# Kernel tuning notes

Measured on AMD Instinct MI355X. Metric: run time of the kernel, lower is better.

## Reference

```python
import jax, jax.numpy as jnp
import numpy as np

H = 16          # num_heads
D = 1024        # in_features
NH = D // H     # per-head dim
EPS = 1e-5


def _ln(x, g, b):
    m = jnp.mean(x, axis=-1, keepdims=True)
    v = jnp.mean((x - m) ** 2, axis=-1, keepdims=True)
    return (x - m) / jnp.sqrt(v + EPS) * g + b


def _mha(q, k, v, Wq, bq, Wk, bk, Wv, bv, causal):
    # q: [Tq,B,D], k/v: [Tk,B,D]
    Tq, B, _ = q.shape
    Tk = k.shape[0]
    qh = (q @ Wq + bq).reshape(Tq, B, H, NH)
    kh = (k @ Wk + bk).reshape(Tk, B, H, NH)
    vh = (v @ Wv + bv).reshape(Tk, B, H, NH)
    scale = 1.0 / np.float32(np.sqrt(NH))
    logits = jnp.einsum('qbhd,kbhd->bhqk', qh, kh) * scale  # [B,H,Tq,Tk]
    if causal:
        mask = jnp.tril(jnp.ones((Tq, Tk), dtype=bool))
        logits = jnp.where(mask, logits, -jnp.inf)  # softmax over prefix [0..t]
    w = jax.nn.softmax(logits, axis=-1)
    out = jnp.einsum('bhqk,kbhd->qbhd', w, vh).reshape(Tq, B, D)
    return out


def setup_inputs() -> dict:
    key = jax.random.key(0)
    ks = jax.random.split(key, 12)
    s = 0.02
    T, B = 1024, 8
    inp = {
        'encoder_input': jax.random.normal(ks[0], (T, B, D), jnp.float32),
        'decoder_input': jax.random.normal(ks[1], (T, B, D), jnp.float32),
        # self-attention projections
        'Wq1': jax.random.normal(ks[2], (D, D), jnp.float32) * s,
        'bq1': jnp.zeros((D,), jnp.float32),
        'Wk1': jax.random.normal(ks[3], (D, D), jnp.float32) * s,
        'bk1': jnp.zeros((D,), jnp.float32),
        'Wv1': jax.random.normal(ks[4], (D, D), jnp.float32) * s,
        'bv1': jnp.zeros((D,), jnp.float32),
        # cross-attention projections
        'Wq2': jax.random.normal(ks[5], (D, D), jnp.float32) * s,
        'bq2': jnp.zeros((D,), jnp.float32),
        'Wk2': jax.random.normal(ks[6], (D, D), jnp.float32) * s,
        'bk2': jnp.zeros((D,), jnp.float32),
        'Wv2': jax.random.normal(ks[7], (D, D), jnp.float32) * s,
        'bv2': jnp.zeros((D,), jnp.float32),
        # position-wise linear
        'Wl': jax.random.normal(ks[8], (D, D), jnp.float32) * s,
        'bl': jnp.zeros((D,), jnp.float32),
        # layernorms
        'g1': jnp.ones((D,), jnp.float32), 'be1': jnp.zeros((D,), jnp.float32),
        'g2': jnp.ones((D,), jnp.float32), 'be2': jnp.zeros((D,), jnp.float32),
        'g3': jnp.ones((D,), jnp.float32), 'be3': jnp.zeros((D,), jnp.float32),
    }
    return inp


def reference(encoder_input, decoder_input,
              Wq1, bq1, Wk1, bk1, Wv1, bv1,
              Wq2, bq2, Wk2, bk2, Wv2, bv2,
              Wl, bl, g1, be1, g2, be2, g3, be3):
    # causal self-attention (prefix [:t+1] per step == causal mask)
    x = _mha(decoder_input, decoder_input, decoder_input,
             Wq1, bq1, Wk1, bk1, Wv1, bv1, causal=True)
    x = _ln(x + decoder_input, g1, be1)
    # cross-attention over full encoder input
    y = _mha(x, encoder_input, encoder_input,
             Wq2, bq2, Wk2, bk2, Wv2, bv2, causal=False)
    y = _ln(y + x, g2, be2)
    # position-wise linear (no activation in source) + residual + LN
    z = y @ Wl + bl
    out = _ln(z + y, g3, be3)
    return out
```

## Files before the change

kernel.cpp:

```cpp
#include <hip/hip_runtime.h>
#include <hip/hip_bf16.h>

typedef __bf16 bf16x8 __attribute__((ext_vector_type(8)));
typedef float f32x4 __attribute__((ext_vector_type(4)));

#define MFMA16(A, B, C) __builtin_amdgcn_mfma_f32_16x16x32_bf16(A, B, C, 0, 0, 0)

#define GLDS(gp, lp)                                                              \
    __builtin_amdgcn_global_load_lds(                                             \
        (const __attribute__((address_space(1))) void*)(gp),                      \
        (__attribute__((address_space(3))) void*)(lp), 16, 0, 0)

struct PtrW { const float* p[7]; };
__global__ __launch_bounds__(256) void wt_transpose(PtrW W, __hip_bfloat16* __restrict__ Wt) {
    const float* __restrict__ src = W.p[blockIdx.z];
    __hip_bfloat16* __restrict__ dst = Wt + ((size_t)blockIdx.z << 20);
    __shared__ float tile[32][33];
    const int bn = blockIdx.x * 32;
    const int bk = blockIdx.y * 32;
    const int tx = threadIdx.x, ty = threadIdx.y;
#pragma unroll
    for (int i = 0; i < 4; i++) {
        tile[ty + i * 8][tx] = src[(size_t)(bk + ty + i * 8) * 1024 + bn + tx];
    }
    __syncthreads();
#pragma unroll
    for (int i = 0; i < 4; i++) {
        dst[(size_t)(bn + ty + i * 8) * 1024 + bk + tx] =
            __float2bfloat16(tile[tx][ty + i * 8]);
    }
}

struct PtrC { const float* s[2]; __hip_bfloat16* d[2]; };
__global__ __launch_bounds__(256) void to_bf16(PtrC c) {
    const int z = blockIdx.y;
    const int i = (blockIdx.x * 256 + threadIdx.x) * 4;
    const float4 v = *(const float4*)(c.s[z] + i);
    __align__(8) __hip_bfloat16 t[4] = {__float2bfloat16(v.x), __float2bfloat16(v.y),
                                        __float2bfloat16(v.z), __float2bfloat16(v.w)};
    *(uint2*)(c.d[z] + i) = *(const uint2*)t;
}

struct Ptr2 { const float* p[2]; };
__global__ __launch_bounds__(256) void bias_concat(Ptr2 srcs, float* __restrict__ dst) {
    const int i = threadIdx.x * 4;
    *(float4*)(dst + blockIdx.x * 1024 + i) = *(const float4*)(srcs.p[blockIdx.x] + i);
}

struct Job {
    const __hip_bfloat16* A;
    const __hip_bfloat16* B;
    const float* bias;
    __hip_bfloat16* out;
    int bstride;
    int N;
    int nblocks;
    int gx;
    float qscale;
    int qcols;
};
struct Jobs { Job j[4]; int njobs; };

__global__ __launch_bounds__(256) void gemm_multi(Jobs J) {
    int bid = blockIdx.x;
    int ji = 0;
    while (ji < J.njobs - 1 && bid >= J.j[ji].nblocks) {
        bid -= J.j[ji].nblocks;
        ji++;
    }
    const Job job = J.j[ji];
    int bx, by, bb;
    if (job.N) {
        bx = bid % job.gx;
        by = bid / job.gx;
        bb = 0;
    } else {
        bx = bid & 7;
        by = (bid >> 3) & 7;
        bb = bid >> 6;
    }
    __shared__ __align__(16) __hip_bfloat16 As[2][128 * 32];
    __shared__ __align__(16) __hip_bfloat16 Bs[2][128 * 32];
    const int tid = threadIdx.x;
    const int wave = tid >> 6, lane = tid & 63;
    const int quad = lane >> 4, l16 = lane & 15;
    const int m0 = bx * 128, n0 = by * 128;
    const int wm = (wave & 1) * 64, wn = (wave >> 1) * 64;
    const int srow = lane >> 2;
    const int lc = (lane & 3) ^ ((lane >> 3) & 3);
    const __hip_bfloat16* Bbase = job.B + (job.N ? 0 : bb * 1024);
    const __hip_bfloat16* ap[2];
    const __hip_bfloat16* bp[2];
    int loff[2];
#pragma unroll
    for (int u = 0; u < 2; u++) {
        const int g = wave * 2 + u;
        const int row = g * 16 + srow;
        ap[u] = job.A + (size_t)(m0 + row) * 1024 + lc * 8;
        bp[u] = Bbase + (size_t)(n0 + row) * job.bstride + lc * 8;
        loff[u] = g * 512;
    }
    const int pch = quad ^ ((l16 >> 1) & 3);
    f32x4 acc[4][4] = {};
#pragma unroll
    for (int u = 0; u < 2; u++) {
        GLDS(ap[u], &As[0][loff[u]]);
        GLDS(bp[u], &Bs[0][loff[u]]);
    }
    int sel = 0;
    for (int k0 = 0; k0 < 1024; k0 += 32) {
        __syncthreads();
        if (k0 + 32 < 1024) {
#pragma unroll
            for (int u = 0; u < 2; u++) {
                GLDS(ap[u] + k0 + 32, &As[sel ^ 1][loff[u]]);
                GLDS(bp[u] + k0 + 32, &Bs[sel ^ 1][loff[u]]);
            }
        }
        bf16x8 af[4], bfr[4];
#pragma unroll
        for (int i = 0; i < 4; i++) {
            af[i] = *(const bf16x8*)(&As[sel][(wm + i * 16 + l16) * 32 + pch * 8]);
            bfr[i] = *(const bf16x8*)(&Bs[sel][(wn + i * 16 + l16) * 32 + pch * 8]);
        }
#pragma unroll
        for (int i = 0; i < 4; i++)
#pragma unroll
            for (int j = 0; j < 4; j++)
                acc[i][j] = MFMA16(af[i], bfr[j], acc[i][j]);
        sel ^= 1;
    }
    if (job.N) {
#pragma unroll
        for (int i = 0; i < 4; i++) {
#pragma unroll
            for (int j = 0; j < 4; j++) {
                const int mr = m0 + wm + i * 16 + quad * 4;
                const int nc = n0 + wn + j * 16 + l16;
                const float sc = (nc < job.qcols) ? job.qscale : 1.0f;
                const float bv = job.bias[nc];
#pragma unroll
                for (int r = 0; r < 4; r++) {
                    const float v = (acc[i][j][r] + bv) * sc;
                    job.out[(size_t)(mr + r) * job.N + nc] = __float2bfloat16(v);
                }
            }
        }
    } else {
#pragma unroll
        for (int i = 0; i < 4; i++) {
            const int mr = m0 + wm + i * 16 + quad * 4;
            float bias_r[4];
#pragma unroll
            for (int r = 0; r < 4; r++) bias_r[r] = job.bias[mr + r];
#pragma unroll
            for (int j = 0; j < 4; j++) {
                const int nc = n0 + wn + j * 16 + l16;
#pragma unroll
                for (int r = 0; r < 4; r++) {
                    const int d = mr + r;
                    const size_t idx = ((size_t)bb << 20) + ((size_t)(d >> 6) << 16) +
                                       (size_t)(d & 63) * 1024 + nc;
                    job.out[idx] = __float2bfloat16(acc[i][j][r] + bias_r[r]);
                }
            }
        }
    }
}

__global__ __launch_bounds__(256) void attn_kernel(
    const __hip_bfloat16* __restrict__ Qp, const __hip_bfloat16* __restrict__ Kp,
    const __hip_bfloat16* __restrict__ Vt, __hip_bfloat16* __restrict__ Ob,
    int T, int qRS, int kRS, int causal) {
    __shared__ __align__(16) __hip_bfloat16 Ks[2][64 * 64];
    __shared__ __align__(16) __hip_bfloat16 Vs[2][64 * 64];
    __shared__ __align__(16) __hip_bfloat16 Ps[4][16 * 64];
    const int tid = threadIdx.x, wave = tid >> 6, lane = tid & 63;
    const int quad = lane >> 4, l16 = lane & 15;
    const int gid = blockIdx.x;
    const int bh = (gid & 7) * 16 + ((gid >> 3) & 15);
    const int qt = gid >> 7;
    const int b = bh & 7, h = bh >> 3;
    const int q0 = qt * 128;
    const int qstride = 8 * qRS, kstride = 8 * kRS;
    const int sw = l16 & 7;

    const int qg0 = q0 + wave * 16;
    const int qg1 = qg0 + 64;
    const int myq0 = qg0 + l16, myq1 = qg1 + l16;
    const __hip_bfloat16* qbase = Qp + (size_t)b * qRS + h * 64;
    const bf16x8 qf00 = *(const bf16x8*)(qbase + (size_t)myq0 * qstride + quad * 8);
    const bf16x8 qf01 = *(const bf16x8*)(qbase + (size_t)myq0 * qstride + 32 + quad * 8);
    const bf16x8 qf10 = *(const bf16x8*)(qbase + (size_t)myq1 * qstride + quad * 8);
    const bf16x8 qf11 = *(const bf16x8*)(qbase + (size_t)myq1 * qstride + 32 + quad * 8);
    bf16x8 onesf;
#pragma unroll
    for (int i = 0; i < 8; i++) onesf[i] = (__bf16)1.0f;

    const int jk = wave * 2;
    const int lrow = lane >> 3;
    const int lch = (lane & 7) ^ (lrow & 7);
    const __hip_bfloat16* kp0 =
        Kp + (size_t)b * kRS + h * 64 + (size_t)(jk * 8 + lrow) * kstride + lch * 8;
    const __hip_bfloat16* kp1 = kp0 + (size_t)8 * kstride;
    const __hip_bfloat16* vp0 =
        Vt + ((size_t)(b * 16 + h) << 16) + (size_t)(jk * 8 + lrow) * 1024 + lch * 8;
    const __hip_bfloat16* vp1 = vp0 + 8 * 1024;
    const size_t kinc = (size_t)64 * kstride;

    f32x4 o0[4] = {}, o1[4] = {};
    f32x4 ol0 = {}, ol1 = {};
    bf16x8 pf00, pf01, pf10, pf11;

    auto softmax = [&](f32x4* s, f32x4& ol, bf16x8& pf0, bf16x8& pf1, int qg, int myq,
                       int k0) {
        const bool nm = causal && (k0 + 63 > qg);
        if (nm) {
#pragma unroll
            for (int n = 0; n < 4; n++)
#pragma unroll
                for (int r = 0; r < 4; r++)
                    if (k0 + n * 16 + quad * 4 + r > myq) s[n][r] = -1e30f;
        }
#pragma unroll
        for (int n = 0; n < 4; n++) {
            const float p0 = __builtin_amdgcn_exp2f(s[n][0]);
            const float p1 = __builtin_amdgcn_exp2f(s[n][1]);
            const float p2 = __builtin_amdgcn_exp2f(s[n][2]);
            const float p3 = __builtin_amdgcn_exp2f(s[n][3]);
            const __hip_bfloat162 pa = __float22bfloat162_rn(make_float2(p0, p1));
            const __hip_bfloat162 pb = __float22bfloat162_rn(make_float2(p2, p3));
            uint2 w;
            w.x = *(const unsigned int*)&pa;
            w.y = *(const unsigned int*)&pb;
            const int gcp = 2 * n + (quad >> 1);
            *(uint2*)(&Ps[wave][l16 * 64 + ((gcp ^ sw) << 3) + (quad & 1) * 4]) = w;
        }
        pf0 = *(const bf16x8*)(&Ps[wave][l16 * 64 + ((quad ^ sw) << 3)]);
        pf1 = *(const bf16x8*)(&Ps[wave][l16 * 64 + (((quad + 4) ^ sw) << 3)]);
        ol = MFMA16(onesf, pf0, ol);
        ol = MFMA16(onesf, pf1, ol);
    };

    const int kend = causal ? (q0 + 128) : T;
    GLDS(kp0, &Ks[0][jk * 512]);
    GLDS(kp1, &Ks[0][jk * 512 + 512]);
    GLDS(vp0, &Vs[0][jk * 512]);
    GLDS(vp1, &Vs[0][jk * 512 + 512]);
    const __hip_bfloat16* kn0 = kp0 + kinc;
    const __hip_bfloat16* kn1 = kp1 + kinc;
    const __hip_bfloat16* vn0 = vp0 + 64;
    const __hip_bfloat16* vn1 = vp1 + 64;
    int sel = 0;
    for (int k0 = 0; k0 < kend; k0 += 64) {
        __syncthreads();
        if (k0 + 64 < kend) {
            GLDS(kn0, &Ks[sel ^ 1][jk * 512]);
            GLDS(kn1, &Ks[sel ^ 1][jk * 512 + 512]);
            GLDS(vn0, &Vs[sel ^ 1][jk * 512]);
            GLDS(vn1, &Vs[sel ^ 1][jk * 512 + 512]);
            kn0 += kinc; kn1 += kinc; vn0 += 64; vn1 += 64;
        }
        const bool act0 = !causal || (k0 <= qg0 + 15);
        f32x4 s0[4] = {}, s1[4] = {};
        {
            bf16x8 kf[4];
#pragma unroll
            for (int n = 0; n < 4; n++)
                kf[n] = *(const bf16x8*)(&Ks[sel][(n * 16 + l16) * 64 +
                                                  ((quad ^ sw) << 3)]);
#pragma unroll
            for (int n = 0; n < 4; n++) {
                if (act0) s0[n] = MFMA16(kf[n], qf00, s0[n]);
                s1[n] = MFMA16(kf[n], qf10, s1[n]);
            }
#pragma unroll
            for (int n = 0; n < 4; n++)
                kf[n] = *(const bf16x8*)(&Ks[sel][(n * 16 + l16) * 64 +
                                                  (((quad + 4) ^ sw) << 3)]);
#pragma unroll
            for (int n = 0; n < 4; n++) {
                if (act0) s0[n] = MFMA16(kf[n], qf01, s0[n]);
                s1[n] = MFMA16(kf[n], qf11, s1[n]);
            }
        }
        if (act0) softmax(s0, ol0, pf00, pf01, qg0, myq0, k0);
        softmax(s1, ol1, pf10, pf11, qg1, myq1, k0);
#pragma unroll
        for (int mm = 0; mm < 4; mm++) {
            const int vrow = (mm * 16 + l16) * 64;
            const bf16x8 vf0 = *(const bf16x8*)(&Vs[sel][vrow + ((quad ^ sw) << 3)]);
            const bf16x8 vf1 = *(const bf16x8*)(&Vs[sel][vrow + (((quad + 4) ^ sw) << 3)]);
            if (act0) {
                o0[mm] = MFMA16(vf0, pf00, o0[mm]);
                o0[mm] = MFMA16(vf1, pf01, o0[mm]);
            }
            o1[mm] = MFMA16(vf0, pf10, o1[mm]);
            o1[mm] = MFMA16(vf1, pf11, o1[mm]);
        }
        sel ^= 1;
    }
    const float inv0 = 1.0f / ol0[0];
    const float inv1 = 1.0f / ol1[0];
    __hip_bfloat16* ob0 = Ob + (size_t)b * 1024 + h * 64 + (size_t)myq0 * 8192;
    __hip_bfloat16* ob1 = Ob + (size_t)b * 1024 + h * 64 + (size_t)myq1 * 8192;
#pragma unroll
    for (int mm = 0; mm < 4; mm++) {
        __align__(8) __hip_bfloat16 t0[4] = {
            __float2bfloat16(o0[mm][0] * inv0), __float2bfloat16(o0[mm][1] * inv0),
            __float2bfloat16(o0[mm][2] * inv0), __float2bfloat16(o0[mm][3] * inv0)};
        *(uint2*)(ob0 + mm * 16 + quad * 4) = *(const uint2*)t0;
        __align__(8) __hip_bfloat16 t1[4] = {
            __float2bfloat16(o1[mm][0] * inv1), __float2bfloat16(o1[mm][1] * inv1),
            __float2bfloat16(o1[mm][2] * inv1), __float2bfloat16(o1[mm][3] * inv1)};
        *(uint2*)(ob1 + mm * 16 + quad * 4) = *(const uint2*)t1;
    }
}

__global__ __launch_bounds__(256) void ln_res_kernel(
    const __hip_bfloat16* __restrict__ a, const float* __restrict__ resf,
    const __hip_bfloat16* __restrict__ resb, const float* __restrict__ g,
    const float* __restrict__ be, float* __restrict__ outf,
    __hip_bfloat16* __restrict__ outb) {
    const int tid = threadIdx.x, wave = tid >> 6, lane = tid & 63;
    const int row = blockIdx.x * 4 + wave;
    const size_t base = (size_t)row * 1024;
    float x[16];
#pragma unroll
    for (int c = 0; c < 4; c++) {
        const int off = c * 256 + lane * 4;
        const uint2 ar = *(const uint2*)(a + base + off);
        const __hip_bfloat16* ah = (const __hip_bfloat16*)&ar;
        if (resf) {
            const float4 rv = *(const float4*)(resf + base + off);
            x[c * 4 + 0] = __bfloat162float(ah[0]) + rv.x;
            x[c * 4 + 1] = __bfloat162float(ah[1]) + rv.y;
            x[c * 4 + 2] = __bfloat162float(ah[2]) + rv.z;
            x[c * 4 + 3] = __bfloat162float(ah[3]) + rv.w;
        } else {
            const uint2 br = *(const uint2*)(resb + base + off);
            const __hip_bfloat16* bhp = (const __hip_bfloat16*)&br;
#pragma unroll
            for (int k = 0; k < 4; k++)
                x[c * 4 + k] = __bfloat162float(ah[k]) + __bfloat162float(bhp[k]);
        }
    }
    float s = 0.f, ss = 0.f;
#pragma unroll
    for (int k = 0; k < 16; k++) {
        s += x[k];
        ss += x[k] * x[k];
    }
#pragma unroll
    for (int w = 32; w >= 1; w >>= 1) {
        s += __shfl_xor(s, w);
        ss += __shfl_xor(ss, w);
    }
    const float mean = s * (1.f / 1024.f);
    const float inv = rsqrtf(ss * (1.f / 1024.f) - mean * mean + 1e-5f);
#pragma unroll
    for (int c = 0; c < 4; c++) {
        const int off = c * 256 + lane * 4;
        const float4 gg = *(const float4*)(g + off);
        const float4 bb = *(const float4*)(be + off);
        float y[4];
        y[0] = (x[c * 4 + 0] - mean) * inv * gg.x + bb.x;
        y[1] = (x[c * 4 + 1] - mean) * inv * gg.y + bb.y;
        y[2] = (x[c * 4 + 2] - mean) * inv * gg.z + bb.z;
        y[3] = (x[c * 4 + 3] - mean) * inv * gg.w + bb.w;
        if (outf) *(float4*)(outf + base + off) = make_float4(y[0], y[1], y[2], y[3]);
        if (outb) {
            __align__(8) __hip_bfloat16 t[4] = {
                __float2bfloat16(y[0]), __float2bfloat16(y[1]),
                __float2bfloat16(y[2]), __float2bfloat16(y[3])};
            *(uint2*)(outb + base + off) = *(const uint2*)t;
        }
    }
}

extern "C" void kernel_launch(void* const* d_in, const int* in_sizes, int n_in,
                              void* d_out, int out_size, void* d_ws, size_t ws_size,
                              hipStream_t stream) {
    const float* enc = (const float*)d_in[0];
    const float* dec = (const float*)d_in[1];
    const float* Wq1 = (const float*)d_in[2];
    const float* bq1 = (const float*)d_in[3];
    const float* Wk1 = (const float*)d_in[4];
    const float* bk1 = (const float*)d_in[5];
    const float* Wv1 = (const float*)d_in[6];
    const float* bv1 = (const float*)d_in[7];
    const float* Wq2 = (const float*)d_in[8];
    const float* bq2 = (const float*)d_in[9];
    const float* Wk2 = (const float*)d_in[10];
    const float* bk2 = (const float*)d_in[11];
    const float* Wv2 = (const float*)d_in[12];
    const float* bv2 = (const float*)d_in[13];
    const float* Wl = (const float*)d_in[14];
    const float* bl = (const float*)d_in[15];
    const float* g1 = (const float*)d_in[16];
    const float* be1 = (const float*)d_in[17];
    const float* g2 = (const float*)d_in[18];
    const float* be2 = (const float*)d_in[19];
    const float* g3 = (const float*)d_in[20];
    const float* be3 = (const float*)d_in[21];
    float* outp = (float*)d_out;

    char* p = (char*)d_ws;
    auto alloc = [&](size_t n) {
        char* r = p;
        p += (n + 255) & ~(size_t)255;
        return r;
    };
    const size_t MD = (size_t)8192 * 1024;
    __hip_bfloat16* enc_b = (__hip_bfloat16*)alloc(MD * 2);
    __hip_bfloat16* dec_b = (__hip_bfloat16*)alloc(MD * 2);
    __hip_bfloat16* Wt = (__hip_bfloat16*)alloc((size_t)7 * 1024 * 1024 * 2);
    float* bcat = (float*)alloc(2048 * sizeof(float));
    __hip_bfloat16* qk = (__hip_bfloat16*)alloc(MD * 2 * 2);
    __hip_bfloat16* k2b = (__hip_bfloat16*)alloc(MD * 2);
    __hip_bfloat16* qb = (__hip_bfloat16*)alloc(MD * 2);
    __hip_bfloat16* attnb = (__hip_bfloat16*)alloc(MD * 2);
    __hip_bfloat16* Vtb = (__hip_bfloat16*)alloc(MD * 2);
    __hip_bfloat16* Vtb2 = (__hip_bfloat16*)alloc(MD * 2);
    __hip_bfloat16* xb = dec_b;
    __hip_bfloat16* yb = enc_b;

    const float QSC = 0.18033688f;

    PtrW wptrs = {{Wq1, Wk1, Wv1, Wq2, Wk2, Wv2, Wl}};
    wt_transpose<<<dim3(32, 32, 7), dim3(32, 8), 0, stream>>>(wptrs, Wt);
    PtrC cp = {{enc, dec}, {enc_b, dec_b}};
    to_bf16<<<dim3(8192, 2), 256, 0, stream>>>(cp);
    Ptr2 bp = {{bq1, bk1}};
    bias_concat<<<2, 256, 0, stream>>>(bp, bcat);

    {
        Jobs J;
        J.j[0] = {dec_b, Wt, bcat, qk, 1024, 2048, 64 * 16, 64, QSC, 1024};
        J.j[1] = {Wt + ((size_t)2 << 20), dec_b, bv1, Vtb, 8192, 0, 512, 8, 1.0f, 0};
        J.j[2] = {enc_b, Wt + ((size_t)4 << 20), bk2, k2b, 1024, 1024, 64 * 8, 64, 1.0f, 0};
        J.j[3] = {Wt + ((size_t)5 << 20), enc_b, bv2, Vtb2, 8192, 0, 512, 8, 1.0f, 0};
        J.njobs = 4;
        gemm_multi<<<2560, 256, 0, stream>>>(J);
    }

    attn_kernel<<<1024, 256, 0, stream>>>(qk, qk + 1024, Vtb, attnb,
                                          1024, 2048, 2048, 1);
    ln_res_kernel<<<2048, 256, 0, stream>>>(attnb, dec, nullptr, g1, be1, nullptr, xb);

    {
        Jobs J;
        J.j[0] = {xb, Wt + ((size_t)3 << 20), bq2, qb, 1024, 1024, 64 * 8, 64, QSC, 1024};
        J.njobs = 1;
        gemm_multi<<<512, 256, 0, stream>>>(J);
    }
    attn_kernel<<<1024, 256, 0, stream>>>(qb, k2b, Vtb2, attnb, 1024, 1024, 1024, 0);
    ln_res_kernel<<<2048, 256, 0, stream>>>(attnb, nullptr, xb, g2, be2, nullptr, yb);

    {
        Jobs J;
        J.j[0] = {yb, Wt + ((size_t)6 << 20), bl, qb, 1024, 1024, 64 * 8, 64, 1.0f, 0};
        J.njobs = 1;
        gemm_multi<<<512, 256, 0, stream>>>(J);
    }
    ln_res_kernel<<<2048, 256, 0, stream>>>(qb, nullptr, yb, g3, be3, outp, nullptr);
}
```

Baseline: 524.2 us.

## Pair causal query tiles per block and move cross-attn K/V GEMMs later

Result: faster. 499.4 us (-4.7%).

```diff
diff --git a/kernel.cpp b/kernel.cpp
--- a/kernel.cpp
+++ b/kernel.cpp
@@ -59,7 +59,7 @@
     float qscale;
     int qcols;
 };
-struct Jobs { Job j[4]; int njobs; };
+struct Jobs { Job j[3]; int njobs; };
 
 __global__ __launch_bounds__(256) void gemm_multi(Jobs J) {
     int bid = blockIdx.x;
@@ -171,7 +171,7 @@
 __global__ __launch_bounds__(256) void attn_kernel(
     const __hip_bfloat16* __restrict__ Qp, const __hip_bfloat16* __restrict__ Kp,
     const __hip_bfloat16* __restrict__ Vt, __hip_bfloat16* __restrict__ Ob,
-    int T, int qRS, int kRS, int causal) {
+    int T, int qRS, int kRS, int causal, int paired) {
     __shared__ __align__(16) __hip_bfloat16 Ks[2][64 * 64];
     __shared__ __align__(16) __hip_bfloat16 Vs[2][64 * 64];
     __shared__ __align__(16) __hip_bfloat16 Ps[4][16 * 64];
@@ -179,141 +179,146 @@
     const int quad = lane >> 4, l16 = lane & 15;
     const int gid = blockIdx.x;
     const int bh = (gid & 7) * 16 + ((gid >> 3) & 15);
-    const int qt = gid >> 7;
+    const int sid = gid >> 7;
     const int b = bh & 7, h = bh >> 3;
-    const int q0 = qt * 128;
     const int qstride = 8 * qRS, kstride = 8 * kRS;
     const int sw = l16 & 7;
-
-    const int qg0 = q0 + wave * 16;
-    const int qg1 = qg0 + 64;
-    const int myq0 = qg0 + l16, myq1 = qg1 + l16;
-    const __hip_bfloat16* qbase = Qp + (size_t)b * qRS + h * 64;
-    const bf16x8 qf00 = *(const bf16x8*)(qbase + (size_t)myq0 * qstride + quad * 8);
-    const bf16x8 qf01 = *(const bf16x8*)(qbase + (size_t)myq0 * qstride + 32 + quad * 8);
-    const bf16x8 qf10 = *(const bf16x8*)(qbase + (size_t)myq1 * qstride + quad * 8);
-    const bf16x8 qf11 = *(const bf16x8*)(qbase + (size_t)myq1 * qstride + 32 + quad * 8);
-    bf16x8 onesf;
-#pragma unroll
-    for (int i = 0; i < 8; i++) onesf[i] = (__bf16)1.0f;
-
     const int jk = wave * 2;
     const int lrow = lane >> 3;
     const int lch = (lane & 7) ^ (lrow & 7);
-    const __hip_bfloat16* kp0 =
+    const __hip_bfloat16* qbase = Qp + (size_t)b * qRS + h * 64;
+    const __hip_bfloat16* kbase =
         Kp + (size_t)b * kRS + h * 64 + (size_t)(jk * 8 + lrow) * kstride + lch * 8;
-    const __hip_bfloat16* kp1 = kp0 + (size_t)8 * kstride;
-    const __hip_bfloat16* vp0 =
+    const __hip_bfloat16* vbase =
         Vt + ((size_t)(b * 16 + h) << 16) + (size_t)(jk * 8 + lrow) * 1024 + lch * 8;
-    const __hip_bfloat16* vp1 = vp0 + 8 * 1024;
     const size_t kinc = (size_t)64 * kstride;
-
-    f32x4 o0[4] = {}, o1[4] = {};
-    f32x4 ol0 = {}, ol1 = {};
-    bf16x8 pf00, pf01, pf10, pf11;
-
-    auto softmax = [&](f32x4* s, f32x4& ol, bf16x8& pf0, bf16x8& pf1, int qg, int myq,
-                       int k0) {
-        const bool nm = causal && (k0 + 63 > qg);
-        if (nm) {
-#pragma unroll
-            for (int n = 0; n < 4; n++)
-#pragma unroll
-                for (int r = 0; r < 4; r++)
-                    if (k0 + n * 16 + quad * 4 + r > myq) s[n][r] = -1e30f;
-        }
-#pragma unroll
-        for (int n = 0; n < 4; n++) {
-            const float p0 = __builtin_amdgcn_exp2f(s[n][0]);
-            const float p1 = __builtin_amdgcn_exp2f(s[n][1]);
-            const float p2 = __builtin_amdgcn_exp2f(s[n][2]);
-            const float p3 = __builtin_amdgcn_exp2f(s[n][3]);
-            const __hip_bfloat162 pa = __float22bfloat162_rn(make_float2(p0, p1));
-            const __hip_bfloat162 pb = __float22bfloat162_rn(make_float2(p2, p3));
-            uint2 w;
-            w.x = *(const unsigned int*)&pa;
-            w.y = *(const unsigned int*)&pb;
-            const int gcp = 2 * n + (quad >> 1);
-            *(uint2*)(&Ps[wave][l16 * 64 + ((gcp ^ sw) << 3) + (quad & 1) * 4]) = w;
-        }
-        pf0 = *(const bf16x8*)(&Ps[wave][l16 * 64 + ((quad ^ sw) << 3)]);
-        pf1 = *(const bf16x8*)(&Ps[wave][l16 * 64 + (((quad + 4) ^ sw) << 3)]);
-        ol = MFMA16(onesf, pf0, ol);
-        ol = MFMA16(onesf, pf1, ol);
-    };
-
-    const int kend = causal ? (q0 + 128) : T;
-    GLDS(kp0, &Ks[0][jk * 512]);
-    GLDS(kp1, &Ks[0][jk * 512 + 512]);
-    GLDS(vp0, &Vs[0][jk * 512]);
-    GLDS(vp1, &Vs[0][jk * 512 + 512]);
-    const __hip_bfloat16* kn0 = kp0 + kinc;
-    const __hip_bfloat16* kn1 = kp1 + kinc;
-    const __hip_bfloat16* vn0 = vp0 + 64;
-    const __hip_bfloat16* vn1 = vp1 + 64;
-    int sel = 0;
-    for (int k0 = 0; k0 < kend; k0 += 64) {
-        __syncthreads();
-        if (k0 + 64 < kend) {
-            GLDS(kn0, &Ks[sel ^ 1][jk * 512]);
-            GLDS(kn1, &Ks[sel ^ 1][jk * 512 + 512]);
-            GLDS(vn0, &Vs[sel ^ 1][jk * 512]);
-            GLDS(vn1, &Vs[sel ^ 1][jk * 512 + 512]);
-            kn0 += kinc; kn1 += kinc; vn0 += 64; vn1 += 64;
-        }
-        const bool act0 = !causal || (k0 <= qg0 + 15);
-        f32x4 s0[4] = {}, s1[4] = {};
-        {
-            bf16x8 kf[4];
-#pragma unroll
-            for (int n = 0; n < 4; n++)
-                kf[n] = *(const bf16x8*)(&Ks[sel][(n * 16 + l16) * 64 +
-                                                  ((quad ^ sw) << 3)]);
+    bf16x8 onesf;
+#pragma unroll
+    for (int i = 0; i < 8; i++) onesf[i] = (__bf16)1.0f;
+
+    const int nrep = paired ? 2 : 1;
+    for (int rep = 0; rep < nrep; rep++) {
+        const int qt = paired ? (rep ? sid : 7 - sid) : sid;
+        const int q0 = qt * 128;
+        const int qg0 = q0 + wave * 16;
+        const int qg1 = qg0 + 64;
+        const int myq0 = qg0 + l16, myq1 = qg1 + l16;
+        const bf16x8 qf00 = *(const bf16x8*)(qbase + (size_t)myq0 * qstride + quad * 8);
+        const bf16x8 qf01 =
+            *(const bf16x8*)(qbase + (size_t)myq0 * qstride + 32 + quad * 8);
+        const bf16x8 qf10 = *(const bf16x8*)(qbase + (size_t)myq1 * qstride + quad * 8);
+        const bf16x8 qf11 =
+            *(const bf16x8*)(qbase + (size_t)myq1 * qstride + 32 + quad * 8);
+
+        f32x4 o0[4] = {}, o1[4] = {};
+        f32x4 ol0 = {}, ol1 = {};
+        bf16x8 pf00, pf01, pf10, pf11;
+
+        auto softmax = [&](f32x4* s, f32x4& ol, bf16x8& pf0, bf16x8& pf1, int qg,
+                           int myq, int k0) {
+            const bool nm = causal && (k0 + 63 > qg);
+            if (nm) {
+#pragma unroll
+                for (int n = 0; n < 4; n++)
+#pragma unroll
+                    for (int r = 0; r < 4; r++)
+                        if (k0 + n * 16 + quad * 4 + r > myq) s[n][r] = -1e30f;
+            }
 #pragma unroll
             for (int n = 0; n < 4; n++) {
-                if (act0) s0[n] = MFMA16(kf[n], qf00, s0[n]);
-                s1[n] = MFMA16(kf[n], qf10, s1[n]);
-            }
-#pragma unroll
-            for (int n = 0; n < 4; n++)
-                kf[n] = *(const bf16x8*)(&Ks[sel][(n * 16 + l16) * 64 +
-                                                  (((quad + 4) ^ sw) << 3)]);
-#pragma unroll
-            for (int n = 0; n < 4; n++) {
-                if (act0) s0[n] = MFMA16(kf[n], qf01, s0[n]);
-                s1[n] = MFMA16(kf[n], qf11, s1[n]);
-            }
-        }
-        if (act0) softmax(s0, ol0, pf00, pf01, qg0, myq0, k0);
-        softmax(s1, ol1, pf10, pf11, qg1, myq1, k0);
+                const float p0 = __builtin_amdgcn_exp2f(s[n][0]);
+                const float p1 = __builtin_amdgcn_exp2f(s[n][1]);
+                const float p2 = __builtin_amdgcn_exp2f(s[n][2]);
+                const float p3 = __builtin_amdgcn_exp2f(s[n][3]);
+                const __hip_bfloat162 pa = __float22bfloat162_rn(make_float2(p0, p1));
+                const __hip_bfloat162 pb = __float22bfloat162_rn(make_float2(p2, p3));
+                uint2 w;
+                w.x = *(const unsigned int*)&pa;
+                w.y = *(const unsigned int*)&pb;
+                const int gcp = 2 * n + (quad >> 1);
+                *(uint2*)(&Ps[wave][l16 * 64 + ((gcp ^ sw) << 3) + (quad & 1) * 4]) = w;
+            }
+            pf0 = *(const bf16x8*)(&Ps[wave][l16 * 64 + ((quad ^ sw) << 3)]);
+            pf1 = *(const bf16x8*)(&Ps[wave][l16 * 64 + (((quad + 4) ^ sw) << 3)]);
+            ol = MFMA16(onesf, pf0, ol);
+            ol = MFMA16(onesf, pf1, ol);
+        };
+
+        const int kend = causal ? (q0 + 128) : T;
+        if (rep) __syncthreads();
+        GLDS(kbase, &Ks[0][jk * 512]);
+        GLDS(kbase + (size_t)8 * kstride, &Ks[0][jk * 512 + 512]);
+        GLDS(vbase, &Vs[0][jk * 512]);
+        GLDS(vbase + 8 * 1024, &Vs[0][jk * 512 + 512]);
+        const __hip_bfloat16* kn0 = kbase + kinc;
+        const __hip_bfloat16* kn1 = kbase + (size_t)8 * kstride + kinc;
+        const __hip_bfloat16* vn0 = vbase + 64;
+        const __hip_bfloat16* vn1 = vbase + 8 * 1024 + 64;
+        int sel = 0;
+        for (int k0 = 0; k0 < kend; k0 += 64) {
+            __syncthreads();
+            if (k0 + 64 < kend) {
+                GLDS(kn0, &Ks[sel ^ 1][jk * 512]);
+                GLDS(kn1, &Ks[sel ^ 1][jk * 512 + 512]);
+                GLDS(vn0, &Vs[sel ^ 1][jk * 512]);
+                GLDS(vn1, &Vs[sel ^ 1][jk * 512 + 512]);
+                kn0 += kinc; kn1 += kinc; vn0 += 64; vn1 += 64;
+            }
+            const bool act0 = !causal || (k0 <= qg0 + 15);
+            f32x4 s0[4] = {}, s1[4] = {};
+            {
+                bf16x8 kf[4];
+#pragma unroll
+                for (int n = 0; n < 4; n++)
+                    kf[n] = *(const bf16x8*)(&Ks[sel][(n * 16 + l16) * 64 +
+                                                      ((quad ^ sw) << 3)]);
+#pragma unroll
+                for (int n = 0; n < 4; n++) {
+                    if (act0) s0[n] = MFMA16(kf[n], qf00, s0[n]);
+                    s1[n] = MFMA16(kf[n], qf10, s1[n]);
+                }
+#pragma unroll
+                for (int n = 0; n < 4; n++)
+                    kf[n] = *(const bf16x8*)(&Ks[sel][(n * 16 + l16) * 64 +
+                                                      (((quad + 4) ^ sw) << 3)]);
+#pragma unroll
+                for (int n = 0; n < 4; n++) {
+                    if (act0) s0[n] = MFMA16(kf[n], qf01, s0[n]);
+                    s1[n] = MFMA16(kf[n], qf11, s1[n]);
+                }
+            }
+            if (act0) softmax(s0, ol0, pf00, pf01, qg0, myq0, k0);
+            softmax(s1, ol1, pf10, pf11, qg1, myq1, k0);
+#pragma unroll
+            for (int mm = 0; mm < 4; mm++) {
+                const int vrow = (mm * 16 + l16) * 64;
+                const bf16x8 vf0 = *(const bf16x8*)(&Vs[sel][vrow + ((quad ^ sw) << 3)]);
+                const bf16x8 vf1 =
+                    *(const bf16x8*)(&Vs[sel][vrow + (((quad + 4) ^ sw) << 3)]);
+                if (act0) {
+                    o0[mm] = MFMA16(vf0, pf00, o0[mm]);
+                    o0[mm] = MFMA16(vf1, pf01, o0[mm]);
+                }
+                o1[mm] = MFMA16(vf0, pf10, o1[mm]);
+                o1[mm] = MFMA16(vf1, pf11, o1[mm]);
+            }
+            sel ^= 1;
+        }
+        const float inv0 = 1.0f / ol0[0];
+        const float inv1 = 1.0f / ol1[0];
+        __hip_bfloat16* ob0 = Ob + (size_t)b * 1024 + h * 64 + (size_t)myq0 * 8192;
+        __hip_bfloat16* ob1 = Ob + (size_t)b * 1024 + h * 64 + (size_t)myq1 * 8192;
 #pragma unroll
         for (int mm = 0; mm < 4; mm++) {
-            const int vrow = (mm * 16 + l16) * 64;
-            const bf16x8 vf0 = *(const bf16x8*)(&Vs[sel][vrow + ((quad ^ sw) << 3)]);
-            const bf16x8 vf1 = *(const bf16x8*)(&Vs[sel][vrow + (((quad + 4) ^ sw) << 3)]);
-            if (act0) {
-                o0[mm] = MFMA16(vf0, pf00, o0[mm]);
-                o0[mm] = MFMA16(vf1, pf01, o0[mm]);
-            }
-            o1[mm] = MFMA16(vf0, pf10, o1[mm]);
-            o1[mm] = MFMA16(vf1, pf11, o1[mm]);
-        }
-        sel ^= 1;
-    }
-    const float inv0 = 1.0f / ol0[0];
-    const float inv1 = 1.0f / ol1[0];
-    __hip_bfloat16* ob0 = Ob + (size_t)b * 1024 + h * 64 + (size_t)myq0 * 8192;
-    __hip_bfloat16* ob1 = Ob + (size_t)b * 1024 + h * 64 + (size_t)myq1 * 8192;
-#pragma unroll
-    for (int mm = 0; mm < 4; mm++) {
-        __align__(8) __hip_bfloat16 t0[4] = {
-            __float2bfloat16(o0[mm][0] * inv0), __float2bfloat16(o0[mm][1] * inv0),
-            __float2bfloat16(o0[mm][2] * inv0), __float2bfloat16(o0[mm][3] * inv0)};
-        *(uint2*)(ob0 + mm * 16 + quad * 4) = *(const uint2*)t0;
-        __align__(8) __hip_bfloat16 t1[4] = {
-            __float2bfloat16(o1[mm][0] * inv1), __float2bfloat16(o1[mm][1] * inv1),
-            __float2bfloat16(o1[mm][2] * inv1), __float2bfloat16(o1[mm][3] * inv1)};
-        *(uint2*)(ob1 + mm * 16 + quad * 4) = *(const uint2*)t1;
+            __align__(8) __hip_bfloat16 t0[4] = {
+                __float2bfloat16(o0[mm][0] * inv0), __float2bfloat16(o0[mm][1] * inv0),
+                __float2bfloat16(o0[mm][2] * inv0), __float2bfloat16(o0[mm][3] * inv0)};
+            *(uint2*)(ob0 + mm * 16 + quad * 4) = *(const uint2*)t0;
+            __align__(8) __hip_bfloat16 t1[4] = {
+                __float2bfloat16(o1[mm][0] * inv1), __float2bfloat16(o1[mm][1] * inv1),
+                __float2bfloat16(o1[mm][2] * inv1), __float2bfloat16(o1[mm][3] * inv1)};
+            *(uint2*)(ob1 + mm * 16 + quad * 4) = *(const uint2*)t1;
+        }
     }
 }
 
@@ -438,23 +443,24 @@
         Jobs J;
         J.j[0] = {dec_b, Wt, bcat, qk, 1024, 2048, 64 * 16, 64, QSC, 1024};
         J.j[1] = {Wt + ((size_t)2 << 20), dec_b, bv1, Vtb, 8192, 0, 512, 8, 1.0f, 0};
-        J.j[2] = {enc_b, Wt + ((size_t)4 << 20), bk2, k2b, 1024, 1024, 64 * 8, 64, 1.0f, 0};
-        J.j[3] = {Wt + ((size_t)5 << 20), enc_b, bv2, Vtb2, 8192, 0, 512, 8, 1.0f, 0};
-        J.njobs = 4;
-        gemm_multi<<<2560, 256, 0, stream>>>(J);
-    }
-
-    attn_kernel<<<1024, 256, 0, stream>>>(qk, qk + 1024, Vtb, attnb,
-                                          1024, 2048, 2048, 1);
+        J.njobs = 2;
+        gemm_multi<<<1536, 256, 0, stream>>>(J);
+    }
+
+    attn_kernel<<<512, 256, 0, stream>>>(qk, qk + 1024, Vtb, attnb,
+                                         1024, 2048, 2048, 1, 1);
     ln_res_kernel<<<2048, 256, 0, stream>>>(attnb, dec, nullptr, g1, be1, nullptr, xb);
 
     {
         Jobs J;
         J.j[0] = {xb, Wt + ((size_t)3 << 20), bq2, qb, 1024, 1024, 64 * 8, 64, QSC, 1024};
-        J.njobs = 1;
-        gemm_multi<<<512, 256, 0, stream>>>(J);
-    }
-    attn_kernel<<<1024, 256, 0, stream>>>(qb, k2b, Vtb2, attnb, 1024, 1024, 1024, 0);
+        J.j[1] = {enc_b, Wt + ((size_t)4 << 20), bk2, k2b, 1024, 1024, 64 * 8, 64, 1.0f, 0};
+        J.j[2] = {Wt + ((size_t)5 << 20), enc_b, bv2, Vtb2, 8192, 0, 512, 8, 1.0f, 0};
+        J.njobs = 3;
+        gemm_multi<<<1536, 256, 0, stream>>>(J);
+    }
+
+    attn_kernel<<<1024, 256, 0, stream>>>(qb, k2b, Vtb2, attnb, 1024, 1024, 1024, 0, 0);
     ln_res_kernel<<<2048, 256, 0, stream>>>(attnb, nullptr, xb, g2, be2, nullptr, yb);
 
     {
```
